# Kernel tuning notes

Measured on AMD Instinct MI355X. Metric: run time of the kernel, lower is better.

Reference implementation:

```python
import jax, jax.numpy as jnp
import numpy as np

B, N, NVT, HS, NZ = 512, 256, 32, 128, 64


def setup_inputs() -> dict:
    key = jax.random.key(0)
    ks = jax.random.split(key, 16)
    node_types = jax.random.randint(ks[0], (B, N), 0, NVT, dtype=jnp.int32)
    node_types = node_types.at[:, 0].set(0)      # START_TYPE
    node_types = node_types.at[:, -1].set(1)     # END_TYPE
    adj = jax.random.randint(ks[1], (B, N, N), 0, 2, dtype=jnp.int32)
    # DAG: edges only u -> v with u < v (strict upper triangular)
    tri = jnp.triu(jnp.ones((N, N), jnp.int32), k=1)
    adj = adj * tri[None, :, :]
    s = 0.05
    p = lambda k, shp: (jax.random.normal(k, shp, jnp.float32) * s)
    return {
        "node_types": node_types,
        "adj": adj,
        "W_ih": p(ks[2], (3 * HS, NVT)),   # grue_forward weight_ih
        "W_hh": p(ks[3], (3 * HS, HS)),    # grue_forward weight_hh
        "b_ih": p(ks[4], (3 * HS,)),
        "b_hh": p(ks[5], (3 * HS,)),
        "Wg": p(ks[6], (HS, NVT)),         # gate_forward linear
        "bg": p(ks[7], (HS,)),
        "Wm": p(ks[8], (HS, NVT)),         # mapper_forward (no bias)
        "W1": p(ks[9], (NZ, HS)),          # fc1 -> mu
        "b1": p(ks[10], (NZ,)),
        "W2": p(ks[11], (NZ, HS)),         # fc2 -> logvar
        "b2": p(ks[12], (NZ,)),
    }


def reference(node_types, adj, W_ih, W_hh, b_ih, b_hh, Wg, bg, Wm, W1, b1, W2, b2):
    hs = Wg.shape[0]
    # one-hot vertex types  [B, N, nvt]
    X = jax.nn.one_hot(node_types, Wg.shape[1], dtype=W_ih.dtype)
    # gated message from each vertex's TYPE (mapper has no bias -> padding contributes 0)
    gated = jax.nn.sigmoid(jnp.einsum('bnv,hv->bnh', X, Wg) + bg) \
            * jnp.einsum('bnv,hv->bnh', X, Wm)                      # [B, N, hs]
    A = adj.astype(gated.dtype)
    # predecessor aggregation: H_v = sum_{u: u->v} gated_u
    Hpre = jnp.einsum('buv,buh->bvh', A, gated)                     # [B, N, hs]
    # torch GRUCell(X_v, Hpre_v), vectorized over all vertices (no recurrence:
    # messages depend only on predecessor types)
    gi = jnp.einsum('bnv,gv->bng', X, W_ih) + b_ih                  # [B, N, 3hs]
    gh = jnp.einsum('bnh,gh->bng', Hpre, W_hh) + b_hh
    r = jax.nn.sigmoid(gi[..., :hs] + gh[..., :hs])
    z = jax.nn.sigmoid(gi[..., hs:2 * hs] + gh[..., hs:2 * hs])
    n = jnp.tanh(gi[..., 2 * hs:] + r * gh[..., 2 * hs:])
    Hv = (1.0 - z) * n + z * Hpre                                   # H_forward, [B, N, hs]
    # graph state: sum over vertices [1, N-1) (start=1, end_offset=1)
    Hg = Hv[:, 1:-1, :].sum(axis=1)                                 # [B, hs]
    mu = Hg @ W1.T + b1
    logvar = Hg @ W2.T + b2
    return (mu, logvar)
```

## Files before the change

### kernel.cpp

```cpp
#include <hip/hip_runtime.h>
#include <hip/hip_bf16.h>

#define HS 128
#define NVT 32
#define NN 256

typedef __attribute__((ext_vector_type(8))) short bf16x8;
typedef __attribute__((ext_vector_type(4))) float f32x4;

#define TABB_OFF 0
#define GIT_OFF  32768

static __device__ __forceinline__ short f2bs(float f) {
    __hip_bfloat16 h = __float2bfloat16(f);
    short s; __builtin_memcpy(&s, &h, 2);
    return s;
}
static __device__ __forceinline__ float bs2f(short s) {
    __hip_bfloat16 h; __builtin_memcpy(&h, &s, 2);
    return __bfloat162float(h);
}
static __device__ __forceinline__ float sigm(float x) {
    return __builtin_amdgcn_rcpf(1.f + __expf(-x));
}

__global__ void __launch_bounds__(512) build_tables(
    const float* __restrict__ W_ih, const float* __restrict__ W_hh,
    const float* __restrict__ b_ih, const float* __restrict__ b_hh,
    const float* __restrict__ Wg,   const float* __restrict__ bg,
    const float* __restrict__ Wm,
    short* __restrict__ TABB, short* __restrict__ GIT)
{
    __shared__ float G_s[HS];
    const int t = blockIdx.x;
    const int j = threadIdx.x;
    if (j < HS) {
        float x = Wg[j * NVT + t] + bg[j];
        G_s[j] = sigm(x) * Wm[j * NVT + t];
    }
    __syncthreads();
    if (j < 384) {
        float acc = 0.f;
        for (int h = 0; h < HS; ++h) acc += G_s[h] * W_hh[j * HS + h];
        TABB[j * NVT + t] = f2bs(acc);
        float git = W_ih[j * NVT + t] + b_ih[j];
        if (j < 256) git += b_hh[j];
        GIT[t * 384 + j] = f2bs(git);
    } else {
        TABB[j * NVT + t] = f2bs(G_s[j - 384]);
    }
}

__global__ void __launch_bounds__(512) dvae_fused(
    const int* __restrict__ node_types, const int* __restrict__ adj,
    const short* __restrict__ TABB, const short* __restrict__ GIT,
    const float* __restrict__ b_hh,
    const float* __restrict__ W1, const float* __restrict__ b1,
    const float* __restrict__ W2, const float* __restrict__ b2,
    float* __restrict__ out)
{
    __shared__ unsigned cntA[NN * 20];
    __shared__ short GITs[NVT * 388];
    __shared__ unsigned tmask[NVT * 8];
    __shared__ int types_s[NN];
    __shared__ float hg_s[HS];

    const int b = blockIdx.x, tid = threadIdx.x;
    const int wave = tid >> 6, lane = tid & 63;
    const int quad = lane >> 4, col = lane & 15;

    if (tid < NN) types_s[tid] = node_types[b * NN + tid];

    {
        const unsigned* src = (const unsigned*)GIT;
        unsigned* dst = (unsigned*)GITs;
        #pragma unroll
        for (int c = 0; c < 12; ++c) {
            int i = c * 512 + tid;
            int t = i / 192, j = i - t * 192;
            dst[t * 194 + j] = src[i];
        }
    }

    bf16x8 bfrag[4];
    #pragma unroll
    for (int g = 0; g < 4; ++g) {
        int jb = (g < 3 ? g * 128 : 384) + wave * 16;
        bfrag[g] = *(const bf16x8*)(TABB + (jb + col) * 32 + quad * 8);
    }
    const int h0 = wave * 16 + col;
    const float bhn = b_hh[256 + h0];

    unsigned cb[8];
    if (tid < NN) {
        const int* colp = adj + (size_t)b * NN * NN + tid;
        #pragma unroll
        for (int w8 = 0; w8 < 8; ++w8) {
            int avv[32];
            #pragma unroll
            for (int j = 0; j < 32; ++j) avv[j] = colp[(w8 * 32 + j) * NN];
            unsigned wd = 0;
            #pragma unroll
            for (int j = 0; j < 32; ++j) wd |= ((unsigned)avv[j]) << j;
            cb[w8] = wd;
        }
    }
    __syncthreads();

    if (tid < NN) {
        int t = tid >> 3, w8 = tid & 7;
        unsigned mw = 0;
        #pragma unroll
        for (int k = 0; k < 32; ++k)
            mw |= ((unsigned)(types_s[w8 * 32 + k] == t)) << k;
        tmask[tid] = mw;
    }
    __syncthreads();

    if (tid < NN) {
        #pragma unroll
        for (int tp = 0; tp < 16; ++tp) {
            const uint4* m0p = (const uint4*)&tmask[(2 * tp) * 8];
            const uint4* m1p = (const uint4*)&tmask[(2 * tp + 1) * 8];
            uint4 ma = m0p[0], mb = m0p[1], mc = m1p[0], md = m1p[1];
            unsigned c0 = __popc(cb[0] & ma.x) + __popc(cb[1] & ma.y)
                        + __popc(cb[2] & ma.z) + __popc(cb[3] & ma.w)
                        + __popc(cb[4] & mb.x) + __popc(cb[5] & mb.y)
                        + __popc(cb[6] & mb.z) + __popc(cb[7] & mb.w);
            unsigned c1 = __popc(cb[0] & mc.x) + __popc(cb[1] & mc.y)
                        + __popc(cb[2] & mc.z) + __popc(cb[3] & mc.w)
                        + __popc(cb[4] & md.x) + __popc(cb[5] & md.y)
                        + __popc(cb[6] & md.z) + __popc(cb[7] & md.w);
            unsigned p = (__float_as_uint((float)c0) >> 16)
                       | (__float_as_uint((float)c1) & 0xFFFF0000u);
            cntA[tid * 20 + tp] = p;
        }
    }
    __syncthreads();

    float hg = 0.f;
    for (int m = 0; m < 16; ++m) {
        bf16x8 afrag = *(const bf16x8*)(cntA + (m * 16 + col) * 20 + quad * 4);
        f32x4 acc[4];
        #pragma unroll
        for (int g = 0; g < 4; ++g)
            acc[g] = __builtin_amdgcn_mfma_f32_16x16x32_bf16(
                afrag, bfrag[g], (f32x4){0.f, 0.f, 0.f, 0.f}, 0, 0, 0);
        #pragma unroll
        for (int r = 0; r < 4; ++r) {
            int vv = m * 16 + quad * 4 + r;
            int tv = types_s[vv];
            const short* g = GITs + tv * 388;
            float gir = bs2f(g[h0]);
            float giz = bs2f(g[128 + h0]);
            float gin = bs2f(g[256 + h0]);
            float rr = sigm(gir + acc[0][r]);
            float zz = sigm(giz + acc[1][r]);
            float x2 = gin + rr * (acc[2][r] + bhn);
            float nt = 1.f - 2.f * __builtin_amdgcn_rcpf(1.f + __expf(2.f * x2));
            float msk = (vv >= 1 && vv < NN - 1) ? 1.f : 0.f;
            hg += msk * ((1.f - zz) * nt + zz * acc[3][r]);
        }
    }
    hg += __shfl_xor(hg, 16);
    hg += __shfl_xor(hg, 32);
    if (lane < 16) hg_s[h0] = hg;
    __syncthreads();

    if (tid < 128) {
        int which = tid >> 6, zz = tid & 63;
        const float* W = which ? W2 : W1;
        float acc2 = which ? b2[zz] : b1[zz];
        const float4* Wv = (const float4*)(W + zz * HS);
        #pragma unroll
        for (int i = 0; i < 32; ++i) {
            float4 ww = Wv[i];
            acc2 += hg_s[4 * i] * ww.x + hg_s[4 * i + 1] * ww.y
                  + hg_s[4 * i + 2] * ww.z + hg_s[4 * i + 3] * ww.w;
        }
        out[which * 32768 + b * 64 + zz] = acc2;
    }
}

extern "C" void kernel_launch(void* const* d_in, const int* in_sizes, int n_in,
                              void* d_out, int out_size, void* d_ws, size_t ws_size,
                              hipStream_t stream)
{
    const int* node_types = (const int*)d_in[0];
    const int* adj        = (const int*)d_in[1];
    const float* W_ih = (const float*)d_in[2];
    const float* W_hh = (const float*)d_in[3];
    const float* b_ih = (const float*)d_in[4];
    const float* b_hh = (const float*)d_in[5];
    const float* Wg   = (const float*)d_in[6];
    const float* bg   = (const float*)d_in[7];
    const float* Wm   = (const float*)d_in[8];
    const float* W1   = (const float*)d_in[9];
    const float* b1   = (const float*)d_in[10];
    const float* W2   = (const float*)d_in[11];
    const float* b2   = (const float*)d_in[12];

    char* ws = (char*)d_ws;
    short* TABB = (short*)(ws + TABB_OFF);
    short* GIT  = (short*)(ws + GIT_OFF);
    float* out  = (float*)d_out;

    build_tables<<<dim3(32), dim3(512), 0, stream>>>(W_ih, W_hh, b_ih, b_hh, Wg, bg, Wm, TABB, GIT);
    dvae_fused<<<dim3(512), dim3(512), 0, stream>>>(node_types, adj, TABB, GIT, b_hh, W1, b1, W2, b2, out);
}
```

Measured before the change: 240.1 us.

## Split each graph across two blocks with coalesced int4 adjacency loads and separate readout

Each graph's 256 target vertices are now split across two workgroups (1024 blocks), so each block handles 128 columns. The adjacency matrix is read as row-wise int4 chunks by all 512 threads and packed into 16-bit column masks in shared memory, replacing per-thread strided column reads by only 256 threads. The GI table is interleaved so the r/z/n gates come from one 8-byte global load, which drops the shared-memory copy of the table. Partial graph sums go to workspace and a new small readout kernel does the mu/logvar projection, at the cost of an extra launch and a global round trip.

```diff
diff --git a/kernel.cpp b/kernel.cpp
--- a/kernel.cpp
+++ b/kernel.cpp
@@ -6,10 +6,12 @@
 #define NN 256
 
 typedef __attribute__((ext_vector_type(8))) short bf16x8;
+typedef __attribute__((ext_vector_type(4))) short s16x4;
 typedef __attribute__((ext_vector_type(4))) float f32x4;
 
 #define TABB_OFF 0
 #define GIT_OFF  32768
+#define HGP_OFF  65536
 
 static __device__ __forceinline__ short f2bs(float f) {
     __hip_bfloat16 h = __float2bfloat16(f);
@@ -45,7 +47,7 @@
         TABB[j * NVT + t] = f2bs(acc);
         float git = W_ih[j * NVT + t] + b_ih[j];
         if (j < 256) git += b_hh[j];
-        GIT[t * 384 + j] = f2bs(git);
+        GIT[t * 512 + (j & 127) * 4 + (j >> 7)] = f2bs(git);
     } else {
         TABB[j * NVT + t] = f2bs(G_s[j - 384]);
     }
@@ -55,32 +57,20 @@
     const int* __restrict__ node_types, const int* __restrict__ adj,
     const short* __restrict__ TABB, const short* __restrict__ GIT,
     const float* __restrict__ b_hh,
-    const float* __restrict__ W1, const float* __restrict__ b1,
-    const float* __restrict__ W2, const float* __restrict__ b2,
-    float* __restrict__ out)
-{
-    __shared__ unsigned cntA[NN * 20];
-    __shared__ short GITs[NVT * 388];
+    float* __restrict__ hgpart)
+{
+    __shared__ int types_s[NN];
     __shared__ unsigned tmask[NVT * 8];
-    __shared__ int types_s[NN];
-    __shared__ float hg_s[HS];
-
-    const int b = blockIdx.x, tid = threadIdx.x;
+    __shared__ unsigned short cmask16[16 * 128];
+    __shared__ unsigned cntA[128 * 20];
+
+    const int bid = blockIdx.x;
+    const int b = bid >> 1, vbase = (bid & 1) << 7;
+    const int tid = threadIdx.x;
     const int wave = tid >> 6, lane = tid & 63;
     const int quad = lane >> 4, col = lane & 15;
 
     if (tid < NN) types_s[tid] = node_types[b * NN + tid];
-
-    {
-        const unsigned* src = (const unsigned*)GIT;
-        unsigned* dst = (unsigned*)GITs;
-        #pragma unroll
-        for (int c = 0; c < 12; ++c) {
-            int i = c * 512 + tid;
-            int t = i / 192, j = i - t * 192;
-            dst[t * 194 + j] = src[i];
-        }
-    }
 
     bf16x8 bfrag[4];
     #pragma unroll
@@ -91,19 +81,22 @@
     const int h0 = wave * 16 + col;
     const float bhn = b_hh[256 + h0];
 
-    unsigned cb[8];
-    if (tid < NN) {
-        const int* colp = adj + (size_t)b * NN * NN + tid;
-        #pragma unroll
-        for (int w8 = 0; w8 < 8; ++w8) {
-            int avv[32];
-            #pragma unroll
-            for (int j = 0; j < 32; ++j) avv[j] = colp[(w8 * 32 + j) * NN];
-            unsigned wd = 0;
-            #pragma unroll
-            for (int j = 0; j < 32; ++j) wd |= ((unsigned)avv[j]) << j;
-            cb[w8] = wd;
+    {
+        const int cg = tid & 31, rb = tid >> 5;
+        const int4* ap = (const int4*)(adj + (size_t)b * NN * NN + rb * 16 * NN + vbase) + cg;
+        unsigned m0 = 0, m1 = 0, m2 = 0, m3 = 0;
+        #pragma unroll
+        for (int j = 0; j < 16; ++j) {
+            int4 a = ap[j * (NN / 4)];
+            m0 |= ((unsigned)a.x) << j;
+            m1 |= ((unsigned)a.y) << j;
+            m2 |= ((unsigned)a.z) << j;
+            m3 |= ((unsigned)a.w) << j;
         }
+        uint2 pk;
+        pk.x = m0 | (m1 << 16);
+        pk.y = m2 | (m3 << 16);
+        *(uint2*)&cmask16[rb * 128 + cg * 4] = pk;
     }
     __syncthreads();
 
@@ -117,9 +110,16 @@
     }
     __syncthreads();
 
-    if (tid < NN) {
-        #pragma unroll
-        for (int tp = 0; tp < 16; ++tp) {
+    {
+        const int v = tid & 127, tpg = tid >> 7;
+        unsigned cb[8];
+        #pragma unroll
+        for (int w = 0; w < 8; ++w)
+            cb[w] = (unsigned)cmask16[2 * w * 128 + v]
+                  | ((unsigned)cmask16[(2 * w + 1) * 128 + v] << 16);
+        #pragma unroll
+        for (int k = 0; k < 4; ++k) {
+            int tp = tpg * 4 + k;
             const uint4* m0p = (const uint4*)&tmask[(2 * tp) * 8];
             const uint4* m1p = (const uint4*)&tmask[(2 * tp + 1) * 8];
             uint4 ma = m0p[0], mb = m0p[1], mc = m1p[0], md = m1p[1];
@@ -133,13 +133,13 @@
                         + __popc(cb[6] & md.z) + __popc(cb[7] & md.w);
             unsigned p = (__float_as_uint((float)c0) >> 16)
                        | (__float_as_uint((float)c1) & 0xFFFF0000u);
-            cntA[tid * 20 + tp] = p;
+            cntA[v * 20 + tp] = p;
         }
     }
     __syncthreads();
 
     float hg = 0.f;
-    for (int m = 0; m < 16; ++m) {
+    for (int m = 0; m < 8; ++m) {
         bf16x8 afrag = *(const bf16x8*)(cntA + (m * 16 + col) * 20 + quad * 4);
         f32x4 acc[4];
         #pragma unroll
@@ -148,12 +148,12 @@
                 afrag, bfrag[g], (f32x4){0.f, 0.f, 0.f, 0.f}, 0, 0, 0);
         #pragma unroll
         for (int r = 0; r < 4; ++r) {
-            int vv = m * 16 + quad * 4 + r;
+            int vv = vbase + m * 16 + quad * 4 + r;
             int tv = types_s[vv];
-            const short* g = GITs + tv * 388;
-            float gir = bs2f(g[h0]);
-            float giz = bs2f(g[128 + h0]);
-            float gin = bs2f(g[256 + h0]);
+            s16x4 gv = *(const s16x4*)(GIT + tv * 512 + h0 * 4);
+            float gir = bs2f(gv[0]);
+            float giz = bs2f(gv[1]);
+            float gin = bs2f(gv[2]);
             float rr = sigm(gir + acc[0][r]);
             float zz = sigm(giz + acc[1][r]);
             float x2 = gin + rr * (acc[2][r] + bhn);
@@ -164,22 +164,30 @@
     }
     hg += __shfl_xor(hg, 16);
     hg += __shfl_xor(hg, 32);
-    if (lane < 16) hg_s[h0] = hg;
-    __syncthreads();
-
-    if (tid < 128) {
-        int which = tid >> 6, zz = tid & 63;
-        const float* W = which ? W2 : W1;
-        float acc2 = which ? b2[zz] : b1[zz];
-        const float4* Wv = (const float4*)(W + zz * HS);
-        #pragma unroll
-        for (int i = 0; i < 32; ++i) {
-            float4 ww = Wv[i];
-            acc2 += hg_s[4 * i] * ww.x + hg_s[4 * i + 1] * ww.y
-                  + hg_s[4 * i + 2] * ww.z + hg_s[4 * i + 3] * ww.w;
-        }
-        out[which * 32768 + b * 64 + zz] = acc2;
-    }
+    if (lane < 16) hgpart[bid * HS + h0] = hg;
+}
+
+__global__ void __launch_bounds__(128) dvae_readout(
+    const float* __restrict__ hgpart,
+    const float* __restrict__ W1, const float* __restrict__ b1,
+    const float* __restrict__ W2, const float* __restrict__ b2,
+    float* __restrict__ out)
+{
+    __shared__ float hg_s[HS];
+    const int b = blockIdx.x, tid = threadIdx.x;
+    hg_s[tid] = hgpart[(2 * b) * HS + tid] + hgpart[(2 * b + 1) * HS + tid];
+    __syncthreads();
+    const int which = tid >> 6, z = tid & 63;
+    const float* W = which ? W2 : W1;
+    float acc = which ? b2[z] : b1[z];
+    const float4* Wv = (const float4*)(W + z * HS);
+    #pragma unroll
+    for (int i = 0; i < 32; ++i) {
+        float4 ww = Wv[i];
+        acc += hg_s[4 * i] * ww.x + hg_s[4 * i + 1] * ww.y
+             + hg_s[4 * i + 2] * ww.z + hg_s[4 * i + 3] * ww.w;
+    }
+    out[which * 32768 + b * 64 + z] = acc;
 }
 
 extern "C" void kernel_launch(void* const* d_in, const int* in_sizes, int n_in,
@@ -201,10 +209,12 @@
     const float* b2   = (const float*)d_in[12];
 
     char* ws = (char*)d_ws;
-    short* TABB = (short*)(ws + TABB_OFF);
-    short* GIT  = (short*)(ws + GIT_OFF);
-    float* out  = (float*)d_out;
+    short* TABB   = (short*)(ws + TABB_OFF);
+    short* GIT    = (short*)(ws + GIT_OFF);
+    float* hgpart = (float*)(ws + HGP_OFF);
+    float* out    = (float*)d_out;
 
     build_tables<<<dim3(32), dim3(512), 0, stream>>>(W_ih, W_hh, b_ih, b_hh, Wg, bg, Wm, TABB, GIT);
-    dvae_fused<<<dim3(512), dim3(512), 0, stream>>>(node_types, adj, TABB, GIT, b_hh, W1, b1, W2, b2, out);
-}
+    dvae_fused<<<dim3(1024), dim3(512), 0, stream>>>(node_types, adj, TABB, GIT, b_hh, hgpart);
+    dvae_readout<<<dim3(512), dim3(128), 0, stream>>>(hgpart, W1, b1, W2, b2, out);
+}
```

After: 236.9 us. Within noise of the previous version (-1.3%).

## Bit-pack adjacency rows with wave ballots in a separate kernel, transpose in LDS

Applied to the files above, without the earlier changes.

Adds a pre-pass kernel that reads the adjacency matrix row-wise with coalesced 16-byte loads and packs it into 64-bit bitmasks via ballots. It replaces the old strided column reads of the whole int32 matrix inside the main kernel. The main kernel then loads the compact bitmasks, transposes them with a shuffle-based bit transpose, builds type masks with ballots and computes predecessor-type counts with 64-bit popcounts. The GI table is re-laid out so the three gate values for a hidden unit sit together and are read straight from global memory instead of being staged in LDS. This costs an extra launch and a workspace round trip for the packed bits.

```diff
diff --git a/kernel.cpp b/kernel.cpp
--- a/kernel.cpp
+++ b/kernel.cpp
@@ -6,10 +6,13 @@
 #define NN 256
 
 typedef __attribute__((ext_vector_type(8))) short bf16x8;
+typedef __attribute__((ext_vector_type(4))) short s16x4;
 typedef __attribute__((ext_vector_type(4))) float f32x4;
+typedef unsigned long long u64;
 
 #define TABB_OFF 0
 #define GIT_OFF  32768
+#define RBG_OFF  65536
 
 static __device__ __forceinline__ short f2bs(float f) {
     __hip_bfloat16 h = __float2bfloat16(f);
@@ -22,6 +25,12 @@
 }
 static __device__ __forceinline__ float sigm(float x) {
     return __builtin_amdgcn_rcpf(1.f + __expf(-x));
+}
+static __device__ __forceinline__ u64 shflx64(u64 x, int m) {
+    unsigned lo = (unsigned)x, hi = (unsigned)(x >> 32);
+    lo = (unsigned)__shfl_xor((int)lo, m);
+    hi = (unsigned)__shfl_xor((int)hi, m);
+    return ((u64)hi << 32) | lo;
 }
 
 __global__ void __launch_bounds__(512) build_tables(
@@ -45,23 +54,46 @@
         TABB[j * NVT + t] = f2bs(acc);
         float git = W_ih[j * NVT + t] + b_ih[j];
         if (j < 256) git += b_hh[j];
-        GIT[t * 384 + j] = f2bs(git);
+        GIT[t * 512 + (j & 127) * 4 + (j >> 7)] = f2bs(git);
     } else {
         TABB[j * NVT + t] = f2bs(G_s[j - 384]);
     }
 }
 
-__global__ void __launch_bounds__(512) dvae_fused(
-    const int* __restrict__ node_types, const int* __restrict__ adj,
+__global__ void __launch_bounds__(256) dvae_bitpack(
+    const int* __restrict__ adj, u64* __restrict__ rbg)
+{
+    const int lane = threadIdx.x & 63;
+    const int wid = blockIdx.x * 4 + (threadIdx.x >> 6);
+    const uint4* ap = (const uint4*)adj;
+    #pragma unroll 1
+    for (int r = wid; r < 512 * NN; r += 16384) {
+        const int r2 = r + 8192;
+        uint4 a = ap[(size_t)r  * 64 + lane];
+        uint4 c = ap[(size_t)r2 * 64 + lane];
+        u64 a0 = __ballot(a.x), a1 = __ballot(a.y), a2 = __ballot(a.z), a3 = __ballot(a.w);
+        u64 c0 = __ballot(c.x), c1 = __ballot(c.y), c2 = __ballot(c.z), c3 = __ballot(c.w);
+        u64 va = (lane & 2) ? ((lane & 1) ? a3 : a2) : ((lane & 1) ? a1 : a0);
+        u64 vc = (lane & 2) ? ((lane & 1) ? c3 : c2) : ((lane & 1) ? c1 : c0);
+        if (lane < 4) {
+            rbg[((r  >> 8) << 10) + (lane << 8) + (r  & 255)] = va;
+            rbg[((r2 >> 8) << 10) + (lane << 8) + (r2 & 255)] = vc;
+        }
+    }
+}
+
+__global__ void __launch_bounds__(512) dvae_gru2(
+    const int* __restrict__ node_types, const u64* __restrict__ rbg,
     const short* __restrict__ TABB, const short* __restrict__ GIT,
     const float* __restrict__ b_hh,
     const float* __restrict__ W1, const float* __restrict__ b1,
     const float* __restrict__ W2, const float* __restrict__ b2,
     float* __restrict__ out)
 {
-    __shared__ unsigned cntA[NN * 20];
-    __shared__ short GITs[NVT * 388];
-    __shared__ unsigned tmask[NVT * 8];
+    __shared__ u64 RBs[4 * 256];
+    __shared__ u64 Ct[4 * 256];
+    __shared__ u64 Tm[NVT * 4];
+    __shared__ unsigned cntA[256 * 20];
     __shared__ int types_s[NN];
     __shared__ float hg_s[HS];
 
@@ -70,17 +102,8 @@
     const int quad = lane >> 4, col = lane & 15;
 
     if (tid < NN) types_s[tid] = node_types[b * NN + tid];
-
-    {
-        const unsigned* src = (const unsigned*)GIT;
-        unsigned* dst = (unsigned*)GITs;
-        #pragma unroll
-        for (int c = 0; c < 12; ++c) {
-            int i = c * 512 + tid;
-            int t = i / 192, j = i - t * 192;
-            dst[t * 194 + j] = src[i];
-        }
-    }
+    RBs[tid]       = rbg[(size_t)b * 1024 + tid];
+    RBs[tid + 512] = rbg[(size_t)b * 1024 + 512 + tid];
 
     bf16x8 bfrag[4];
     #pragma unroll
@@ -90,51 +113,56 @@
     }
     const int h0 = wave * 16 + col;
     const float bhn = b_hh[256 + h0];
-
-    unsigned cb[8];
-    if (tid < NN) {
-        const int* colp = adj + (size_t)b * NN * NN + tid;
-        #pragma unroll
-        for (int w8 = 0; w8 < 8; ++w8) {
-            int avv[32];
-            #pragma unroll
-            for (int j = 0; j < 32; ++j) avv[j] = colp[(w8 * 32 + j) * NN];
-            unsigned wd = 0;
-            #pragma unroll
-            for (int j = 0; j < 32; ++j) wd |= ((unsigned)avv[j]) << j;
-            cb[w8] = wd;
-        }
-    }
-    __syncthreads();
-
-    if (tid < NN) {
-        int t = tid >> 3, w8 = tid & 7;
-        unsigned mw = 0;
-        #pragma unroll
-        for (int k = 0; k < 32; ++k)
-            mw |= ((unsigned)(types_s[w8 * 32 + k] == t)) << k;
-        tmask[tid] = mw;
-    }
-    __syncthreads();
-
-    if (tid < NN) {
-        #pragma unroll
-        for (int tp = 0; tp < 16; ++tp) {
-            const uint4* m0p = (const uint4*)&tmask[(2 * tp) * 8];
-            const uint4* m1p = (const uint4*)&tmask[(2 * tp + 1) * 8];
-            uint4 ma = m0p[0], mb = m0p[1], mc = m1p[0], md = m1p[1];
-            unsigned c0 = __popc(cb[0] & ma.x) + __popc(cb[1] & ma.y)
-                        + __popc(cb[2] & ma.z) + __popc(cb[3] & ma.w)
-                        + __popc(cb[4] & mb.x) + __popc(cb[5] & mb.y)
-                        + __popc(cb[6] & mb.z) + __popc(cb[7] & mb.w);
-            unsigned c1 = __popc(cb[0] & mc.x) + __popc(cb[1] & mc.y)
-                        + __popc(cb[2] & mc.z) + __popc(cb[3] & mc.w)
-                        + __popc(cb[4] & md.x) + __popc(cb[5] & md.y)
-                        + __popc(cb[6] & md.z) + __popc(cb[7] & md.w);
-            unsigned p = (__float_as_uint((float)c0) >> 16)
-                       | (__float_as_uint((float)c1) & 0xFFFF0000u);
-            cntA[tid * 20 + tp] = p;
-        }
+    __syncthreads();
+
+    if (wave < 4) {
+        int ty = types_s[wave * 64 + lane];
+        u64 myb = 0;
+        #pragma unroll
+        for (int t = 0; t < NVT; ++t) {
+            u64 bb = __ballot(ty == t);
+            if (lane == t) myb = bb;
+        }
+        if (lane < NVT) Tm[lane * 4 + wave] = myb;
+    }
+
+    constexpr u64 TMS[6] = {
+        0x5555555555555555ULL, 0x3333333333333333ULL, 0x0F0F0F0F0F0F0F0FULL,
+        0x00FF00FF00FF00FFULL, 0x0000FFFF0000FFFFULL, 0x00000000FFFFFFFFULL };
+    #pragma unroll
+    for (int k2 = 0; k2 < 2; ++k2) {
+        int id = wave * 2 + k2, i = id >> 2, j = id & 3;
+        u64 x = RBs[j * 256 + i * 64 + lane];
+        #pragma unroll
+        for (int s = 5; s >= 0; --s) {
+            int jj = 1 << s;
+            u64 m = TMS[s];
+            u64 y = shflx64(x, jj);
+            x = (lane & jj) ? ((x & ~m) | ((y >> jj) & m))
+                            : ((x & m) | ((y & m) << jj));
+        }
+        Ct[i * 256 + j * 64 + lane] = x;
+    }
+    __syncthreads();
+
+    {
+        const int cp = tid & 255, tg = tid >> 8;
+        u64 cc0 = Ct[cp], cc1 = Ct[256 + cp], cc2 = Ct[512 + cp], cc3 = Ct[768 + cp];
+        unsigned ow[8];
+        #pragma unroll
+        for (int k = 0; k < 8; ++k) {
+            int tp = tg * 8 + k;
+            const u64* T0 = &Tm[(2 * tp) * 4];
+            const u64* T1 = &Tm[(2 * tp + 1) * 4];
+            unsigned c0 = __popcll(cc0 & T0[0]) + __popcll(cc1 & T0[1])
+                        + __popcll(cc2 & T0[2]) + __popcll(cc3 & T0[3]);
+            unsigned c1 = __popcll(cc0 & T1[0]) + __popcll(cc1 & T1[1])
+                        + __popcll(cc2 & T1[2]) + __popcll(cc3 & T1[3]);
+            ow[k] = (__float_as_uint((float)c0) >> 16)
+                  | (__float_as_uint((float)c1) & 0xFFFF0000u);
+        }
+        *(uint4*)&cntA[cp * 20 + tg * 8]     = *(const uint4*)&ow[0];
+        *(uint4*)&cntA[cp * 20 + tg * 8 + 4] = *(const uint4*)&ow[4];
     }
     __syncthreads();
 
@@ -148,12 +176,13 @@
                 afrag, bfrag[g], (f32x4){0.f, 0.f, 0.f, 0.f}, 0, 0, 0);
         #pragma unroll
         for (int r = 0; r < 4; ++r) {
-            int vv = m * 16 + quad * 4 + r;
+            int cpr = m * 16 + quad * 4 + r;
+            int vv = ((cpr & 63) << 2) | (cpr >> 6);
             int tv = types_s[vv];
-            const short* g = GITs + tv * 388;
-            float gir = bs2f(g[h0]);
-            float giz = bs2f(g[128 + h0]);
-            float gin = bs2f(g[256 + h0]);
+            s16x4 gv = *(const s16x4*)(GIT + tv * 512 + h0 * 4);
+            float gir = bs2f(gv[0]);
+            float giz = bs2f(gv[1]);
+            float gin = bs2f(gv[2]);
             float rr = sigm(gir + acc[0][r]);
             float zz = sigm(giz + acc[1][r]);
             float x2 = gin + rr * (acc[2][r] + bhn);
@@ -203,8 +232,10 @@
     char* ws = (char*)d_ws;
     short* TABB = (short*)(ws + TABB_OFF);
     short* GIT  = (short*)(ws + GIT_OFF);
+    u64*   RBG  = (u64*)(ws + RBG_OFF);
     float* out  = (float*)d_out;
 
+    dvae_bitpack<<<dim3(2048), dim3(256), 0, stream>>>(adj, RBG);
     build_tables<<<dim3(32), dim3(512), 0, stream>>>(W_ih, W_hh, b_ih, b_hh, Wg, bg, Wm, TABB, GIT);
-    dvae_fused<<<dim3(512), dim3(512), 0, stream>>>(node_types, adj, TABB, GIT, b_hh, W1, b1, W2, b2, out);
-}
+    dvae_gru2<<<dim3(512), dim3(512), 0, stream>>>(node_types, RBG, TABB, GIT, b_hh, W1, b1, W2, b2, out);
+}
```

Result: slower. 253.9 us (+5.8%).
